# Performance work log

Measured on AMD Instinct MI355X. Metric: run time of the kernel, lower is better.

## Reference

```python
import jax, jax.numpy as jnp
import numpy as np

B, S, R, E, H = 2, 2048, 128, 2048, 16
D = E // H  # head_dim = 128


def _ste(x, q):
    # straight-through estimator: forward=q, backward=identity
    return x + jax.lax.stop_gradient(q - x)


def quant_weight(w):
    # BitNet b1.58-style ternary weight quantization with mean-abs scale
    scale = jnp.clip(jnp.mean(jnp.abs(w)), 1e-5, None)
    q = jnp.clip(jnp.round(w / scale), -1.0, 1.0) * scale
    return _ste(w, q)


def quant_act(x):
    # per-token 8-bit absmax activation quantization
    s = 127.0 / jnp.clip(jnp.max(jnp.abs(x), axis=-1, keepdims=True), 1e-5, None)
    q = jnp.clip(jnp.round(x * s), -128.0, 127.0) / s
    return _ste(x, q)


def quantized_linear(x, w):
    # dequantized low-bit matmul: Xq @ Wq^T
    return quant_act(x) @ quant_weight(w).T


def setup_inputs() -> dict:
    key = jax.random.key(0)
    ks = jax.random.split(key, 8)
    sc = 1.0 / np.sqrt(E)
    return {
        "x": jax.random.normal(ks[0], (B, S, E), dtype=jnp.float32),
        "reasoning_tokens": jax.random.normal(ks[1], (B, R, E), dtype=jnp.float32),
        "q_w": jax.random.normal(ks[2], (E, E), dtype=jnp.float32) * sc,
        "k_w": jax.random.normal(ks[3], (E, E), dtype=jnp.float32) * sc,
        "v_w": jax.random.normal(ks[4], (E, E), dtype=jnp.float32) * sc,
        "out_w": jax.random.normal(ks[5], (E, E), dtype=jnp.float32) * sc,
        "out_b": jnp.zeros((E,), dtype=jnp.float32),
    }


def _heads(t):
    b, s, _ = t.shape
    return t.reshape(b, s, H, D).transpose(0, 2, 1, 3)  # [B,H,S,D]


def reference(x, reasoning_tokens, q_w, k_w, v_w, out_w, out_b):
    b, s, e = x.shape
    # quantized QKV projections (dequant + matmul)
    q = _heads(quantized_linear(x, q_w))
    k = _heads(quantized_linear(x, k_w))
    v = _heads(quantized_linear(x, v_w))
    # reasoning tokens go through the UNquantized projections (per source)
    rk = _heads(reasoning_tokens @ k_w.T)
    rv = _heads(reasoning_tokens @ v_w.T)
    k = jnp.concatenate([k, rk], axis=2)  # [B,H,S+R,D]
    v = jnp.concatenate([v, rv], axis=2)
    scores = jnp.einsum('bhqd,bhkd->bhqk', q, k) / np.sqrt(D).astype(np.float32)
    attn = jax.nn.softmax(scores, axis=-1)
    o = jnp.einsum('bhqk,bhkd->bhqd', attn, v)
    o = o.transpose(0, 2, 1, 3).reshape(b, s, e)
    return o @ out_w.T + out_b
```

## Files before the change

kernel.cpp:

```cpp
#include <hip/hip_runtime.h>


typedef __bf16 bf16;
typedef __bf16 bf16x4 __attribute__((ext_vector_type(4)));
typedef __bf16 bf16x8 __attribute__((ext_vector_type(8)));
typedef float  f32x4  __attribute__((ext_vector_type(4)));
typedef float  f32x16 __attribute__((ext_vector_type(16)));
typedef int    i32x4  __attribute__((ext_vector_type(4)));
typedef char   char8  __attribute__((ext_vector_type(8)));

#define B_   2
#define S_   2048
#define R_   128
#define E_   2048
#define H_   16
#define D_   128
#define NKV  2176
#define HKV  1088
#define NTOK 4096
#define KDIM 2048

typedef const __attribute__((address_space(1))) void* gas_ptr;
typedef __attribute__((address_space(3))) void*       las_ptr;

__device__ __forceinline__ void load_lds16(const void* g, void* l) {
  __builtin_amdgcn_global_load_lds((gas_ptr)g, (las_ptr)l, 16, 0, 0);
}

__global__ __launch_bounds__(256) void abs_sum_k(
    const float* __restrict__ w0, const float* __restrict__ w1,
    const float* __restrict__ w2, double* wsD) {
  int z = blockIdx.y;
  const float* w = z == 0 ? w0 : (z == 1 ? w1 : w2);
  int tid = threadIdx.x;
  size_t base = ((size_t)blockIdx.x * 256 + tid) * 8;
  f32x4 a = *(const f32x4*)(w + base);
  f32x4 b = *(const f32x4*)(w + base + 4);
  float s = 0.f;
#pragma unroll
  for (int j = 0; j < 4; j++) s += fabsf(a[j]) + fabsf(b[j]);
  double d = (double)s;
#pragma unroll
  for (int m = 1; m < 64; m <<= 1) d += __shfl_xor(d, m);
  __shared__ double red[4];
  if ((tid & 63) == 0) red[tid >> 6] = d;
  __syncthreads();
  if (tid == 0) atomicAdd(&wsD[z], red[0] + red[1] + red[2] + red[3]);
}

__global__ __launch_bounds__(256) void prep_k(
    const float* __restrict__ qw, const float* __restrict__ kw,
    const float* __restrict__ vw, const float* __restrict__ ow,
    const float* __restrict__ rt, const double* __restrict__ wsD, float* wsF,
    char* __restrict__ TQ8, char* __restrict__ TK8, char* __restrict__ TV8,
    bf16* __restrict__ KWb, bf16* __restrict__ VWb, bf16* __restrict__ OWb,
    bf16* __restrict__ RTb) {
  int y = blockIdx.y;
  if (y < 3) {
    const float* w = y == 0 ? qw : (y == 1 ? kw : vw);
    char* t        = y == 0 ? TQ8 : (y == 1 ? TK8 : TV8);
    float scale = (float)fmax(wsD[y] * (1.0 / 4194304.0), 1e-5);
    if (blockIdx.x == 0 && threadIdx.x == 0) wsF[y] = scale;
    size_t base = ((size_t)blockIdx.x * 256 + threadIdx.x) * 8;
    f32x4 a = *(const f32x4*)(w + base);
    f32x4 b = *(const f32x4*)(w + base + 4);
    float rs = 1.0f / scale;
    char8 o;
#pragma unroll
    for (int j = 0; j < 8; j++) {
      float v = j < 4 ? a[j] : b[j - 4];
      float q = rintf(v * rs);
      q = fminf(fmaxf(q, -1.f), 1.f);
      o[j] = (char)(int)q;
    }
    *(char8*)(t + base) = o;
  } else {
    if (y == 6 && blockIdx.x >= 256) return;
    const float* src = y == 3 ? kw : (y == 4 ? vw : (y == 5 ? ow : rt));
    bf16* dst        = y == 3 ? KWb : (y == 4 ? VWb : (y == 5 ? OWb : RTb));
    size_t i = ((size_t)blockIdx.x * 256 + threadIdx.x) * 8;
    f32x4 a = *(const f32x4*)(src + i);
    f32x4 b = *(const f32x4*)(src + i + 4);
    bf16x8 o;
#pragma unroll
    for (int j = 0; j < 4; j++) { o[j] = (bf16)a[j]; o[j + 4] = (bf16)b[j]; }
    *(bf16x8*)(dst + i) = o;
  }
}

__global__ __launch_bounds__(256) void actq_k(
    const float* __restrict__ x, char* __restrict__ xq,
    float* __restrict__ aScale) {
  int row = blockIdx.x, tid = threadIdx.x;
  const float* xr = x + (size_t)row * E_;
  f32x4 a = *(const f32x4*)(xr + tid * 8);
  f32x4 b = *(const f32x4*)(xr + tid * 8 + 4);
  float am = 0.f;
#pragma unroll
  for (int j = 0; j < 4; j++) am = fmaxf(am, fmaxf(fabsf(a[j]), fabsf(b[j])));
#pragma unroll
  for (int m = 1; m < 64; m <<= 1) am = fmaxf(am, __shfl_xor(am, m));
  __shared__ float red[4];
  if ((tid & 63) == 0) red[tid >> 6] = am;
  __syncthreads();
  float mx = fmaxf(fmaxf(red[0], red[1]), fmaxf(red[2], red[3]));
  float maxC = fmaxf(mx, 1e-5f);
  float s = 127.0f / maxC;
  char8 o;
#pragma unroll
  for (int j = 0; j < 8; j++) {
    float v = j < 4 ? a[j] : b[j - 4];
    float q = rintf(v * s);
    q = fminf(fmaxf(q, -128.f), 127.f);
    o[j] = (char)(int)q;
  }
  *(char8*)(xq + (size_t)row * E_ + tid * 8) = o;
  if (tid == 0) aScale[row] = maxC / 127.0f;
}

__device__ __forceinline__ void gemm_core(const bf16* Arow, const bf16* Brow,
                                          bf16* As, bf16* Bs, int tid,
                                          f32x4 acc[4][4]) {
  int wave = tid >> 6, lane = tid & 63, quad = lane >> 4, l16 = lane & 15;
  int wm = wave >> 1, wn = wave & 1;
  const char* aT = (const char*)Arow;
  const char* bT = (const char*)Brow;
  int c1 = tid + 256;
  size_t aO0 = (size_t)(tid >> 2) * (KDIM * 2) + (size_t)(tid & 3) * 16;
  size_t aO1 = (size_t)(c1 >> 2) * (KDIM * 2) + (size_t)(c1 & 3) * 16;
  char* AsB = (char*)As;
  char* BsB = (char*)Bs;
  int wofs = wave * 1024;
  for (int k0 = 0; k0 < KDIM; k0 += 32) {
    __syncthreads();
    load_lds16(aT + aO0, AsB + wofs);
    load_lds16(aT + aO1, AsB + 4096 + wofs);
    load_lds16(bT + aO0, BsB + wofs);
    load_lds16(bT + aO1, BsB + 4096 + wofs);
    aT += 64;
    bT += 64;
    __syncthreads();
    bf16x8 af[4], bfr[4];
#pragma unroll
    for (int mt = 0; mt < 4; mt++)
      af[mt] = *(const bf16x8*)(As + (wm * 64 + mt * 16 + l16) * 32 + quad * 8);
#pragma unroll
    for (int nt = 0; nt < 4; nt++)
      bfr[nt] = *(const bf16x8*)(Bs + (wn * 64 + nt * 16 + l16) * 32 + quad * 8);
#pragma unroll
    for (int mt = 0; mt < 4; mt++)
#pragma unroll
      for (int nt = 0; nt < 4; nt++)
        acc[mt][nt] = __builtin_amdgcn_mfma_f32_16x16x32_bf16(
            af[mt], bfr[nt], acc[mt][nt], 0, 0, 0);
  }
}

__device__ __forceinline__ void gemm_core_i8(const char* Arow, const char* Brow,
                                             char* As, char* Bs, int tid,
                                             i32x4 acc[4][4]) {
  int wave = tid >> 6, lane = tid & 63, quad = lane >> 4, l16 = lane & 15;
  int wm = wave >> 1, wn = wave & 1;
  int s0 = tid, s1 = tid + 256;
  int r0 = s0 >> 2, r1 = s1 >> 2;
  size_t aO0 = (size_t)r0 * KDIM + (size_t)((s0 & 3) ^ (r0 & 3)) * 16;
  size_t aO1 = (size_t)r1 * KDIM + (size_t)((s1 & 3) ^ (r1 & 3)) * 16;
  const char* aT = Arow;
  const char* bT = Brow;
  int wofs = wave * 1024;
  int cs = (quad ^ (l16 & 3)) * 16;
  for (int k0 = 0; k0 < KDIM; k0 += 64) {
    __syncthreads();
    load_lds16(aT + aO0, As + wofs);
    load_lds16(aT + aO1, As + 4096 + wofs);
    load_lds16(bT + aO0, Bs + wofs);
    load_lds16(bT + aO1, Bs + 4096 + wofs);
    aT += 64;
    bT += 64;
    __syncthreads();
    i32x4 af[4], bfr[4];
#pragma unroll
    for (int mt = 0; mt < 4; mt++)
      af[mt] = *(const i32x4*)(As + (wm * 64 + mt * 16 + l16) * 64 + cs);
#pragma unroll
    for (int nt = 0; nt < 4; nt++)
      bfr[nt] = *(const i32x4*)(Bs + (wn * 64 + nt * 16 + l16) * 64 + cs);
#pragma unroll
    for (int mt = 0; mt < 4; mt++)
#pragma unroll
      for (int nt = 0; nt < 4; nt++)
        acc[mt][nt] = __builtin_amdgcn_mfma_i32_16x16x64_i8(
            af[mt], bfr[nt], acc[mt][nt], 0, 0, 0);
  }
}

__global__ __launch_bounds__(256) void gemm_proj(
    const char* __restrict__ XQ8, const char* __restrict__ TQ8,
    const char* __restrict__ TK8, const char* __restrict__ TV8,
    const bf16* __restrict__ RTb, const bf16* __restrict__ KWb,
    const bf16* __restrict__ VWb, const float* __restrict__ asc,
    const float* __restrict__ wsF, bf16* __restrict__ QB,
    bf16* __restrict__ KB, bf16* __restrict__ VT) {
  __shared__ char As[8192];
  __shared__ char Bs[8192];
  int tid = threadIdx.x;
  int lane = tid & 63, quad = lane >> 4, l16 = lane & 15;
  int wm = (tid >> 6) >> 1, wn = (tid >> 6) & 1;

  if (blockIdx.y < 32) {
    int m0 = blockIdx.x * 128, n0 = blockIdx.y * 128;
    bool isQ = n0 < 2048;
    bool isRsn = m0 >= NTOK;
    if (isQ && isRsn) return;
    if (!isRsn) {
      const char* Bm = isQ ? (TQ8 + (size_t)n0 * KDIM)
                           : (TK8 + (size_t)(n0 - 2048) * KDIM);
      float sW = isQ ? wsF[0] : wsF[1];
      i32x4 acc[4][4];
      const i32x4 iz = {0, 0, 0, 0};
#pragma unroll
      for (int i = 0; i < 4; i++)
#pragma unroll
        for (int j = 0; j < 4; j++) acc[i][j] = iz;
      gemm_core_i8(XQ8 + (size_t)m0 * KDIM, Bm, As, Bs, tid, acc);
#pragma unroll
      for (int mt = 0; mt < 4; mt++) {
        int mB = m0 + wm * 64 + mt * 16 + quad * 4;
#pragma unroll
        for (int nt = 0; nt < 4; nt++) {
          int n = n0 + wn * 64 + nt * 16 + l16;
          int nn = n & 2047, h = nn >> 7, d = nn & 127;
#pragma unroll
          for (int r = 0; r < 4; r++) {
            int m = mB + r;
            float v = (float)acc[mt][nt][r] * asc[m] * sW;
            int tb = m >> 11, ts = m & 2047;
            if (isQ)
              QB[((size_t)((tb * 16 + h) * S_ + ts)) * 128 + d] = (bf16)v;
            else
              KB[((size_t)((tb * 16 + h) * NKV + ts)) * 128 + d] = (bf16)v;
          }
        }
      }
    } else {
      f32x4 acc[4][4];
      const f32x4 fz = {0.f, 0.f, 0.f, 0.f};
#pragma unroll
      for (int i = 0; i < 4; i++)
#pragma unroll
        for (int j = 0; j < 4; j++) acc[i][j] = fz;
      gemm_core(RTb + (size_t)(m0 - NTOK) * KDIM,
                KWb + (size_t)(n0 - 2048) * KDIM, (bf16*)As, (bf16*)Bs, tid,
                acc);
#pragma unroll
      for (int mt = 0; mt < 4; mt++) {
        int mB = m0 + wm * 64 + mt * 16 + quad * 4;
#pragma unroll
        for (int nt = 0; nt < 4; nt++) {
          int n = n0 + wn * 64 + nt * 16 + l16;
          int nn = n & 2047, h = nn >> 7, d = nn & 127;
#pragma unroll
          for (int r = 0; r < 4; r++) {
            int j = mB + r - NTOK;
            int tb = j >> 7, ts = 2048 + (j & 127);
            KB[((size_t)((tb * 16 + h) * NKV + ts)) * 128 + d] =
                (bf16)acc[mt][nt][r];
          }
        }
      }
    }
  } else {
    int m0 = (blockIdx.y - 32) * 128, n0 = blockIdx.x * 128;
    bool isRsn = n0 >= NTOK;
    if (!isRsn) {
      i32x4 acc[4][4];
      const i32x4 iz = {0, 0, 0, 0};
#pragma unroll
      for (int i = 0; i < 4; i++)
#pragma unroll
        for (int j = 0; j < 4; j++) acc[i][j] = iz;
      gemm_core_i8(TV8 + (size_t)m0 * KDIM, XQ8 + (size_t)n0 * KDIM, As, Bs,
                   tid, acc);
#pragma unroll
      for (int mt = 0; mt < 4; mt++) {
        int mB = m0 + wm * 64 + mt * 16 + quad * 4;
#pragma unroll
        for (int nt = 0; nt < 4; nt++) {
          int n = n0 + wn * 64 + nt * 16 + l16;
          float sb = asc[n] * wsF[2];
          int tb = n >> 11, ts = n & 2047;
#pragma unroll
          for (int r = 0; r < 4; r++) {
            int m = mB + r, h = m >> 7, d = m & 127;
            VT[((size_t)((tb * 16 + h) * 128 + d)) * NKV + ts] =
                (bf16)((float)acc[mt][nt][r] * sb);
          }
        }
      }
    } else {
      f32x4 acc[4][4];
      const f32x4 fz = {0.f, 0.f, 0.f, 0.f};
#pragma unroll
      for (int i = 0; i < 4; i++)
#pragma unroll
        for (int j = 0; j < 4; j++) acc[i][j] = fz;
      gemm_core(VWb + (size_t)m0 * KDIM, RTb + (size_t)(n0 - NTOK) * KDIM,
                (bf16*)As, (bf16*)Bs, tid, acc);
#pragma unroll
      for (int mt = 0; mt < 4; mt++) {
        int mB = m0 + wm * 64 + mt * 16 + quad * 4;
#pragma unroll
        for (int nt = 0; nt < 4; nt++) {
          int n = n0 + wn * 64 + nt * 16 + l16;
          int j = n - NTOK, tb = j >> 7, ts = 2048 + (j & 127);
#pragma unroll
          for (int r = 0; r < 4; r++) {
            int m = mB + r, h = m >> 7, d = m & 127;
            VT[((size_t)((tb * 16 + h) * 128 + d)) * NKV + ts] =
                (bf16)acc[mt][nt][r];
          }
        }
      }
    }
  }
}

__global__ __launch_bounds__(256) void gemm_out(
    const bf16* __restrict__ A, const bf16* __restrict__ Bm,
    const float* __restrict__ bias, float* __restrict__ out) {
  __shared__ bf16 As[128 * 32];
  __shared__ bf16 Bs[128 * 32];
  int m0 = blockIdx.x * 128, n0 = blockIdx.y * 128;
  int tid = threadIdx.x;
  int lane = tid & 63, quad = lane >> 4, l16 = lane & 15;
  int wm = (tid >> 6) >> 1, wn = (tid >> 6) & 1;

  f32x4 acc[4][4];
  const f32x4 fz = {0.f, 0.f, 0.f, 0.f};
#pragma unroll
  for (int i = 0; i < 4; i++)
#pragma unroll
    for (int j = 0; j < 4; j++) acc[i][j] = fz;
  gemm_core(A + (size_t)m0 * KDIM, Bm + (size_t)n0 * KDIM, As, Bs, tid, acc);

#pragma unroll
  for (int mt = 0; mt < 4; mt++) {
    int mB = m0 + wm * 64 + mt * 16 + quad * 4;
#pragma unroll
    for (int nt = 0; nt < 4; nt++) {
      int n = n0 + wn * 64 + nt * 16 + l16;
      float bv = bias[n];
#pragma unroll
      for (int r = 0; r < 4; r++)
        out[(size_t)(mB + r) * E_ + n] = acc[mt][nt][r] + bv;
    }
  }
}

__global__ __launch_bounds__(256) void attn_k(
    const bf16* __restrict__ q, const bf16* __restrict__ k,
    const bf16* __restrict__ vt, bf16* __restrict__ Op,
    float* __restrict__ lp) {
  __shared__ bf16 Ks[64 * 128];
  __shared__ bf16 Vs[128 * 64];
  const float SC = 0.08838834764831845f;
  const float SHIFT = 12.0f;
  int tid = threadIdx.x;
  int wave = tid >> 6, lane = tid & 63, hh = lane >> 5, l31 = lane & 31;
  int bh = blockIdx.y, q0 = blockIdx.x * 128;
  int kv0 = blockIdx.z * HKV;

  const bf16* qb = q + ((size_t)bh * S_ + q0 + wave * 32 + l31) * D_;
  const char* kb = (const char*)(k + (size_t)bh * NKV * D_);
  const char* vb = (const char*)(vt + (size_t)bh * D_ * NKV);

  bf16x8 qf[8];
#pragma unroll
  for (int ds = 0; ds < 8; ds++)
    qf[ds] = *(const bf16x8*)(qb + ds * 16 + hh * 8);

  f32x16 oa[4];
#pragma unroll
  for (int i = 0; i < 4; i++)
#pragma unroll
    for (int r = 0; r < 16; r++) oa[i][r] = 0.f;
  float lsum = 0.f;

  char* KsB = (char*)Ks;
  char* VsB = (char*)Vs;

  int kRow[4], kC[4], vRow[4], vC[4];
#pragma unroll
  for (int i = 0; i < 4; i++) {
    int slot = i * 256 + tid;
    kRow[i] = slot >> 4;
    kC[i] = (slot & 15) ^ (kRow[i] & 15);
    vRow[i] = slot >> 3;
    vC[i] = (slot & 7) ^ (vRow[i] & 7);
  }
  int wofs = wave * 1024;

  for (int kv = kv0; kv < kv0 + HKV; kv += 64) {
    __syncthreads();
#pragma unroll
    for (int i = 0; i < 4; i++)
      load_lds16(kb + (size_t)(kv + kRow[i]) * 256 + kC[i] * 16,
                 KsB + i * 4096 + wofs);
#pragma unroll
    for (int i = 0; i < 4; i++)
      load_lds16(vb + (size_t)vRow[i] * (NKV * 2) + (size_t)kv * 2 + vC[i] * 16,
                 VsB + i * 4096 + wofs);
    __syncthreads();

#pragma unroll
    for (int kb2 = 0; kb2 < 2; kb2++) {
      f32x16 st;
#pragma unroll
      for (int r = 0; r < 16; r++) st[r] = 0.f;
      int krow = kb2 * 32 + l31;
#pragma unroll
      for (int ds = 0; ds < 8; ds++) {
        int c0 = ds * 2 + hh;
        bf16x8 kf = *(const bf16x8*)(KsB + krow * 256 +
                                     ((c0 ^ (krow & 15)) * 16));
        st = __builtin_amdgcn_mfma_f32_32x32x16_bf16(kf, qf[ds], st, 0, 0, 0);
      }
      union {
        bf16 b[16];
        int w[8];
      } pu;
#pragma unroll
      for (int r = 0; r < 16; r++) {
        float e = __expf(st[r] * SC - SHIFT);
        lsum += e;
        pu.b[r] = (bf16)e;
      }
#pragma unroll
      for (int w16 = 0; w16 < 2; w16++) {
        int w0 = pu.w[4 * w16 + 0], w1 = pu.w[4 * w16 + 1];
        int w2 = pu.w[4 * w16 + 2], w3 = pu.w[4 * w16 + 3];
        int s0 = __shfl_xor(w0, 32), s1 = __shfl_xor(w1, 32);
        int s2 = __shfl_xor(w2, 32), s3 = __shfl_xor(w3, 32);
        union {
          int w[4];
          bf16x8 v;
        } fu;
        fu.w[0] = hh ? s2 : w0;
        fu.w[1] = hh ? s3 : w1;
        fu.w[2] = hh ? w2 : s0;
        fu.w[3] = hh ? w3 : s1;
#pragma unroll
        for (int db = 0; db < 4; db++) {
          int vrow = db * 32 + l31;
          int c0 = kb2 * 4 + w16 * 2 + hh;
          bf16x8 vf = *(const bf16x8*)(VsB + vrow * 128 +
                                       ((c0 ^ (vrow & 7)) * 16));
          oa[db] = __builtin_amdgcn_mfma_f32_32x32x16_bf16(vf, fu.v, oa[db],
                                                           0, 0, 0);
        }
      }
    }
  }

  float lred = lsum + __shfl_xor(lsum, 32);
  size_t zofs = (size_t)blockIdx.z * ((size_t)B_ * H_ * S_);
  size_t rbase = zofs + (size_t)bh * S_ + q0 + wave * 32 + l31;
  if (lane < 32) lp[rbase] = lred;
#pragma unroll
  for (int db = 0; db < 4; db++)
#pragma unroll
    for (int g = 0; g < 4; g++) {
      int d = 8 * g + 4 * hh + 32 * db;
      bf16x4 o4;
#pragma unroll
      for (int r = 0; r < 4; r++) o4[r] = (bf16)oa[db][4 * g + r];
      *(bf16x4*)(Op + rbase * 128 + d) = o4;
    }
}

__global__ __launch_bounds__(256) void combine_k(
    const bf16* __restrict__ Op, const float* __restrict__ lp,
    bf16* __restrict__ OB) {
  int m = blockIdx.x, t = threadIdx.x;
  int b = m >> 11, s = m & 2047;
  int idx = t * 8, h = idx >> 7, d = idx & 127;
  size_t rofs = ((size_t)(b * 16 + h) * S_ + s);
  const size_t Z = (size_t)B_ * H_ * S_;
  float rl = 1.0f / (lp[rofs] + lp[Z + rofs]);
  bf16x8 o0 = *(const bf16x8*)(Op + rofs * 128 + d);
  bf16x8 o1 = *(const bf16x8*)(Op + (Z + rofs) * 128 + d);
  bf16x8 o;
#pragma unroll
  for (int j = 0; j < 8; j++) o[j] = (bf16)(((float)o0[j] + (float)o1[j]) * rl);
  *(bf16x8*)(OB + (size_t)m * E_ + idx) = o;
}

static constexpr size_t O_ASC = 256;
static constexpr size_t O_XQ8 = 32768;
static constexpr size_t O_RTB = O_XQ8 + 8388608;
static constexpr size_t O_TQ8 = O_RTB + 1048576;
static constexpr size_t O_TK8 = O_TQ8 + 4194304;
static constexpr size_t O_TV8 = O_TK8 + 4194304;
static constexpr size_t O_KWB = O_TV8 + 4194304;
static constexpr size_t O_VWB = O_KWB + 8388608;
static constexpr size_t O_OWB = O_VWB + 8388608;
static constexpr size_t O_QB  = O_OWB + 8388608;
static constexpr size_t O_KB  = O_QB + 16777216;
static constexpr size_t O_VT  = O_KB + 17825792;
static constexpr size_t WS_NEED = O_VT + 17825792;
static constexpr size_t O_OP = O_XQ8;
static constexpr size_t O_LP = O_XQ8 + 33554432;
static constexpr size_t O_OB = O_QB;

extern "C" void kernel_launch(void* const* d_in, const int* in_sizes, int n_in,
                              void* d_out, int out_size, void* d_ws,
                              size_t ws_size, hipStream_t stream) {
  const float* x  = (const float*)d_in[0];
  const float* rt = (const float*)d_in[1];
  const float* qw = (const float*)d_in[2];
  const float* kw = (const float*)d_in[3];
  const float* vw = (const float*)d_in[4];
  const float* ow = (const float*)d_in[5];
  const float* ob = (const float*)d_in[6];
  char* ws = (char*)d_ws;
  if (ws_size < WS_NEED) return;

  double* wsD = (double*)ws;
  float* wsF  = (float*)(ws + 64);
  float* asc  = (float*)(ws + O_ASC);
  char* XQ8 = ws + O_XQ8;
  bf16* RTb = (bf16*)(ws + O_RTB);
  char* TQ8 = ws + O_TQ8;
  char* TK8 = ws + O_TK8;
  char* TV8 = ws + O_TV8;
  bf16* KWb = (bf16*)(ws + O_KWB);
  bf16* VWb = (bf16*)(ws + O_VWB);
  bf16* OWb = (bf16*)(ws + O_OWB);
  bf16* QB  = (bf16*)(ws + O_QB);
  bf16* KB  = (bf16*)(ws + O_KB);
  bf16* VT  = (bf16*)(ws + O_VT);
  bf16* Op  = (bf16*)(ws + O_OP);
  float* lp = (float*)(ws + O_LP);
  bf16* OB  = (bf16*)(ws + O_OB);
  float* out = (float*)d_out;

  hipMemsetAsync(ws, 0, 64, stream);
  abs_sum_k<<<dim3(2048, 3), 256, 0, stream>>>(qw, kw, vw, wsD);
  prep_k<<<dim3(2048, 7), 256, 0, stream>>>(qw, kw, vw, ow, rt, wsD, wsF,
                                            TQ8, TK8, TV8, KWb, VWb, OWb, RTb);
  actq_k<<<4096, 256, 0, stream>>>(x, XQ8, asc);

  gemm_proj<<<dim3(34, 48), 256, 0, stream>>>(XQ8, TQ8, TK8, TV8, RTb, KWb,
                                              VWb, asc, wsF, QB, KB, VT);

  attn_k<<<dim3(16, 32, 2), 256, 0, stream>>>(QB, KB, VT, Op, lp);
  combine_k<<<4096, 256, 0, stream>>>(Op, lp, OB);

  gemm_out<<<dim3(32, 16), 256, 0, stream>>>(OB, OWb, ob, out);
}
```

Baseline: 523.8 us.

## Drop split-KV attention and combine kernel; normalize output in attention epilogue

The attention kernel now walks the full KV range in one block instead of splitting it in two across blockIdx.z. It normalizes by the row sum directly and writes the result in [B,S,E] layout, which removes the combine kernel and its partial-output and row-sum round trip through memory. Launch bounds now request 4 blocks per CU. The grid shrinks from 1024 to 512 blocks, so fewer blocks are in flight on a GPU with many CUs, and each block runs twice as long.

```diff
diff --git a/kernel.cpp b/kernel.cpp
--- a/kernel.cpp
+++ b/kernel.cpp
@@ -16,7 +16,6 @@
 #define H_   16
 #define D_   128
 #define NKV  2176
-#define HKV  1088
 #define NTOK 4096
 #define KDIM 2048
 
@@ -357,10 +356,9 @@
   }
 }
 
-__global__ __launch_bounds__(256) void attn_k(
+__global__ __launch_bounds__(256, 4) void attn_k(
     const bf16* __restrict__ q, const bf16* __restrict__ k,
-    const bf16* __restrict__ vt, bf16* __restrict__ Op,
-    float* __restrict__ lp) {
+    const bf16* __restrict__ vt, bf16* __restrict__ OB) {
   __shared__ bf16 Ks[64 * 128];
   __shared__ bf16 Vs[128 * 64];
   const float SC = 0.08838834764831845f;
@@ -368,7 +366,6 @@
   int tid = threadIdx.x;
   int wave = tid >> 6, lane = tid & 63, hh = lane >> 5, l31 = lane & 31;
   int bh = blockIdx.y, q0 = blockIdx.x * 128;
-  int kv0 = blockIdx.z * HKV;
 
   const bf16* qb = q + ((size_t)bh * S_ + q0 + wave * 32 + l31) * D_;
   const char* kb = (const char*)(k + (size_t)bh * NKV * D_);
@@ -400,7 +397,7 @@
   }
   int wofs = wave * 1024;
 
-  for (int kv = kv0; kv < kv0 + HKV; kv += 64) {
+  for (int kv = 0; kv < NKV; kv += 64) {
     __syncthreads();
 #pragma unroll
     for (int i = 0; i < 4; i++)
@@ -463,9 +460,10 @@
   }
 
   float lred = lsum + __shfl_xor(lsum, 32);
-  size_t zofs = (size_t)blockIdx.z * ((size_t)B_ * H_ * S_);
-  size_t rbase = zofs + (size_t)bh * S_ + q0 + wave * 32 + l31;
-  if (lane < 32) lp[rbase] = lred;
+  float rl = 1.0f / lred;
+  int b = bh >> 4, h = bh & 15;
+  int s = q0 + wave * 32 + l31;
+  size_t obase = ((size_t)(b * S_ + s)) * E_ + h * 128;
 #pragma unroll
   for (int db = 0; db < 4; db++)
 #pragma unroll
@@ -473,26 +471,9 @@
       int d = 8 * g + 4 * hh + 32 * db;
       bf16x4 o4;
 #pragma unroll
-      for (int r = 0; r < 4; r++) o4[r] = (bf16)oa[db][4 * g + r];
-      *(bf16x4*)(Op + rbase * 128 + d) = o4;
+      for (int r = 0; r < 4; r++) o4[r] = (bf16)(oa[db][4 * g + r] * rl);
+      *(bf16x4*)(OB + obase + d) = o4;
     }
-}
-
-__global__ __launch_bounds__(256) void combine_k(
-    const bf16* __restrict__ Op, const float* __restrict__ lp,
-    bf16* __restrict__ OB) {
-  int m = blockIdx.x, t = threadIdx.x;
-  int b = m >> 11, s = m & 2047;
-  int idx = t * 8, h = idx >> 7, d = idx & 127;
-  size_t rofs = ((size_t)(b * 16 + h) * S_ + s);
-  const size_t Z = (size_t)B_ * H_ * S_;
-  float rl = 1.0f / (lp[rofs] + lp[Z + rofs]);
-  bf16x8 o0 = *(const bf16x8*)(Op + rofs * 128 + d);
-  bf16x8 o1 = *(const bf16x8*)(Op + (Z + rofs) * 128 + d);
-  bf16x8 o;
-#pragma unroll
-  for (int j = 0; j < 8; j++) o[j] = (bf16)(((float)o0[j] + (float)o1[j]) * rl);
-  *(bf16x8*)(OB + (size_t)m * E_ + idx) = o;
 }
 
 static constexpr size_t O_ASC = 256;
@@ -508,9 +489,7 @@
 static constexpr size_t O_KB  = O_QB + 16777216;
 static constexpr size_t O_VT  = O_KB + 17825792;
 static constexpr size_t WS_NEED = O_VT + 17825792;
-static constexpr size_t O_OP = O_XQ8;
-static constexpr size_t O_LP = O_XQ8 + 33554432;
-static constexpr size_t O_OB = O_QB;
+static constexpr size_t O_OB = O_XQ8;
 
 extern "C" void kernel_launch(void* const* d_in, const int* in_sizes, int n_in,
                               void* d_out, int out_size, void* d_ws,
@@ -539,8 +518,6 @@
   bf16* QB  = (bf16*)(ws + O_QB);
   bf16* KB  = (bf16*)(ws + O_KB);
   bf16* VT  = (bf16*)(ws + O_VT);
-  bf16* Op  = (bf16*)(ws + O_OP);
-  float* lp = (float*)(ws + O_LP);
   bf16* OB  = (bf16*)(ws + O_OB);
   float* out = (float*)d_out;
 
@@ -553,8 +530,7 @@
   gemm_proj<<<dim3(34, 48), 256, 0, stream>>>(XQ8, TQ8, TK8, TV8, RTb, KWb,
                                               VWb, asc, wsF, QB, KB, VT);
 
-  attn_k<<<dim3(16, 32, 2), 256, 0, stream>>>(QB, KB, VT, Op, lp);
-  combine_k<<<4096, 256, 0, stream>>>(Op, lp, OB);
+  attn_k<<<dim3(16, 32), 256, 0, stream>>>(QB, KB, VT, OB);
 
   gemm_out<<<dim3(32, 16), 256, 0, stream>>>(OB, OWb, ob, out);
 }
```

New measurement: 623.9 us. 19.1% more time.
